# Performance work log

Hardware: AMD Instinct MI355X
Metric: run time of the kernel (lower is better)

## Reference

```python
import jax, jax.numpy as jnp
import numpy as np

N = 769  # last row is dropped inside forward (per original code)
REPEL_MARGIN = 0.08
MIN_SIZE = 0.02
SIZE_WEIGHT = 1.0
IOU_WEIGHT = 1.0
IOU_MARGIN = 0.1
EPS = 1e-12


def setup_inputs() -> dict:
    key = jax.random.key(0)
    k1, k2, k3 = jax.random.split(key, 3)
    centers = jax.random.uniform(k1, (N, 2), dtype=jnp.float32)
    wh = jax.random.uniform(k2, (N, 2), dtype=jnp.float32) * 0.1 + 0.01
    ang = jax.random.uniform(k3, (N,), dtype=jnp.float32) * np.float32(np.pi) - np.float32(np.pi / 2)
    pred = jnp.concatenate(
        [centers, wh, jnp.cos(ang)[:, None], jnp.sin(ang)[:, None]], axis=-1
    )  # [N, 6] = (cx, cy, w, h, cos_t, sin_t)
    return {"pred": pred}


def _cross(a, b):
    return a[..., 0] * b[..., 1] - a[..., 1] * b[..., 0]


def _corners(b):
    # b [..., 5] = (cx, cy, w, h, theta) -> [..., 4, 2] corners in CCW order
    cx, cy, w, h, a = (b[..., i] for i in range(5))
    c, s = jnp.cos(a), jnp.sin(a)
    dx = jnp.stack([-w, w, w, -w], -1) * 0.5
    dy = jnp.stack([-h, -h, h, h], -1) * 0.5
    x = cx[..., None] + c[..., None] * dx - s[..., None] * dy
    y = cy[..., None] + s[..., None] * dx + c[..., None] * dy
    return jnp.stack([x, y], -1)


def _points_in_box(pts, box):
    # pts [..., 4, 2], box [..., 5] -> bool [..., 4]
    cx, cy, w, h, a = (box[..., i] for i in range(5))
    c, s = jnp.cos(a), jnp.sin(a)
    dx = pts[..., 0] - cx[..., None]
    dy = pts[..., 1] - cy[..., None]
    lx = c[..., None] * dx + s[..., None] * dy
    ly = -s[..., None] * dx + c[..., None] * dy
    return (jnp.abs(lx) <= w[..., None] * 0.5) & (jnp.abs(ly) <= h[..., None] * 0.5)


def box_iou_rotated(boxes):
    # exact pairwise rotated-box IoU, boxes [n, 5] -> [n, n]
    n = boxes.shape[0]
    cor = _corners(boxes)  # [n, 4, 2]
    c1 = jnp.broadcast_to(cor[:, None], (n, n, 4, 2))
    c2 = jnp.broadcast_to(cor[None, :], (n, n, 4, 2))
    # all 4x4 edge-edge intersection candidates
    p = c1[:, :, :, None, :]
    r = (jnp.roll(c1, -1, axis=2) - c1)[:, :, :, None, :]
    q = c2[:, :, None, :, :]
    s = (jnp.roll(c2, -1, axis=2) - c2)[:, :, None, :, :]
    den = _cross(r, s)                         # [n, n, 4, 4]
    safe = jnp.abs(den) > EPS
    den_s = jnp.where(safe, den, 1.0)
    qp = q - p
    t = jnp.where(safe, _cross(qp, s) / den_s, 0.0)
    u = jnp.where(safe, _cross(qp, r) / den_s, 0.0)
    m_int = safe & (t >= 0) & (t <= 1) & (u >= 0) & (u <= 1)
    pts_int = (p + t[..., None] * r).reshape(n, n, 16, 2)
    m_int = m_int.reshape(n, n, 16)
    # corners of each box contained in the other
    m_21 = _points_in_box(c2, boxes[:, None])  # box2 corners in box1
    m_12 = _points_in_box(c1, boxes[None, :])  # box1 corners in box2
    pts_all = jnp.concatenate([pts_int, c2, c1], axis=2)   # [n, n, 24, 2]
    mask = jnp.concatenate([m_int, m_21, m_12], axis=2)    # [n, n, 24]
    # convex-hull area of valid candidate points via angle sort + shoelace
    cnt = mask.sum(-1)
    mf = mask[..., None].astype(pts_all.dtype)
    mean = (pts_all * mf).sum(2) / jnp.maximum(cnt, 1)[..., None]
    d = pts_all - mean[..., None, :]
    ang = jnp.where(mask, jnp.arctan2(d[..., 1], d[..., 0]), 1e6)  # invalids last
    order = jnp.argsort(ang, axis=-1)
    ps = jnp.take_along_axis(pts_all, order[..., None], axis=2)
    ms = jnp.take_along_axis(mask, order, axis=2)
    first = ps[..., 0:1, :]
    pf = jnp.where(ms[..., None], ps, first)  # pad invalid with first valid (zero cross)
    rel = pf - mean[..., None, :]
    inter = 0.5 * jnp.abs(_cross(rel, jnp.roll(rel, -1, axis=2)).sum(-1))
    area = boxes[:, 2] * boxes[:, 3]
    union = area[:, None] + area[None, :] - inter
    return jnp.where(union > EPS, inter / jnp.maximum(union, EPS), 0.0)


def reference(pred):
    pred = pred[:-1]
    m = pred.shape[0]
    centers = pred[:, :2]
    d2 = ((centers[:, None, :] - centers[None, :, :]) ** 2).sum(-1)
    eye = jnp.eye(m, dtype=bool)
    dist = jnp.sqrt(jnp.where(eye, 1.0, d2))
    off = (~eye).astype(dist.dtype)
    repel_loss = (jnp.maximum(REPEL_MARGIN - dist, 0.0) * off).sum() / (m * (m - 1))
    size_pen = jnp.maximum(MIN_SIZE - pred[:, 2], 0.0) + jnp.maximum(MIN_SIZE - pred[:, 3], 0.0)
    size_loss = size_pen.mean()
    total = repel_loss + SIZE_WEIGHT * size_loss
    theta = jnp.arctan2(pred[:, 5], pred[:, 4])
    obb = jnp.concatenate([pred[:, :4], theta[:, None]], axis=-1)
    ious = box_iou_rotated(obb) - jnp.eye(m, dtype=obb.dtype)
    iou_loss = jnp.maximum(ious - IOU_MARGIN, 0.0).mean()
    total = total + IOU_WEIGHT * iou_loss
    return total
```

## Files before the change

### kernel.cpp

```cpp
#include <hip/hip_runtime.h>

#define M  768
#define HALF (M / 2)
#define REPEL_MARGIN 0.08f
#define MIN_SIZE 0.02f
#define IOU_MARGIN 0.1f
#define NBLOCKS M

__device__ inline float edge_contrib(float px, float py, float qx, float qy,
                                     float W, float H,
                                     float bpx, float bpy, float bqx, float bqy) {
    float dx = qx - px, dy = qy - py;
    dx = (fabsf(dx) < 1e-12f) ? 1e-12f : dx;
    dy = (fabsf(dy) < 1e-12f) ? 1e-12f : dy;
    float rdx = __builtin_amdgcn_rcpf(dx);
    float rdy = __builtin_amdgcn_rcpf(dy);
    float tax = (-W - px) * rdx, tbx = (W - px) * rdx;
    float tay = (-H - py) * rdy, tby = (H - py) * rdy;
    float t0 = fmaxf(fmaxf(fminf(tax, tbx), fminf(tay, tby)), 0.0f);
    float t1 = fminf(fminf(fmaxf(tax, tbx), fmaxf(tay, tby)), 1.0f);
    t1 = fmaxf(t1, t0);
    float bdx = bqx - bpx, bdy = bqy - bpy;
    float sx = bpx + t0 * bdx, sy = bpy + t0 * bdy;
    float ex = bpx + t1 * bdx, ey = bpy + t1 * bdy;
    return sx * ey - sy * ex;
}

__global__ void __launch_bounds__(384)
box_repel_stage1(const float* __restrict__ pred, float* __restrict__ partial) {
    const int r = blockIdx.x;
    const int d = threadIdx.x + 1;
    int j = r + d; if (j >= M) j -= M;

    const float* bi = pred + 6 * r;
    const float cxi = bi[0], cyi = bi[1], wi = bi[2], hi = bi[3];
    const float ci = bi[4], si = bi[5];

    const float* bj = pred + 6 * j;
    const float cxj = bj[0], cyj = bj[1], wj = bj[2], hj = bj[3];
    const float cj = bj[4], sj = bj[5];

    const float rx = cxi - cxj, ry = cyi - cyj;
    const float dist = sqrtf(rx * rx + ry * ry);
    float contrib = fmaxf(REPEL_MARGIN - dist, 0.0f)
                    * (1.0f / ((float)M * (float)(M - 1)));

    const float wa = 0.5f * wi, ha = 0.5f * hi;
    const float wb = 0.5f * wj, hb = 0.5f * hj;
    const float tx =  cj * rx + sj * ry;
    const float ty = -sj * rx + cj * ry;
    const float cc = ci * cj + si * sj;
    const float ss = si * cj - ci * sj;

    const float cw = cc * wa, sw = ss * wa, ch = cc * ha, sh = ss * ha;
    const float ax0 = tx - cw + sh, ay0 = ty - sw - ch;
    const float ax1 = tx + cw + sh, ay1 = ty + sw - ch;
    const float ax2 = tx + cw - sh, ay2 = ty + sw + ch;
    const float ax3 = tx - cw - sh, ay3 = ty - sw + ch;

    const float bx0 = -wb, by0 = -hb;
    const float bx1 =  wb, by1 = -hb;
    const float bx2 =  wb, by2 =  hb;
    const float bx3 = -wb, by3 =  hb;

    #define TOA_X(bx, by) ( cc * ((bx) - tx) + ss * ((by) - ty))
    #define TOA_Y(bx, by) (-ss * ((bx) - tx) + cc * ((by) - ty))
    const float qx0 = TOA_X(bx0, by0), qy0 = TOA_Y(bx0, by0);
    const float qx1 = TOA_X(bx1, by1), qy1 = TOA_Y(bx1, by1);
    const float qx2 = TOA_X(bx2, by2), qy2 = TOA_Y(bx2, by2);
    const float qx3 = TOA_X(bx3, by3), qy3 = TOA_Y(bx3, by3);
    #undef TOA_X
    #undef TOA_Y

    float s2 = 0.0f;
    s2 += edge_contrib(ax0, ay0, ax1, ay1, wb, hb, ax0, ay0, ax1, ay1);
    s2 += edge_contrib(ax1, ay1, ax2, ay2, wb, hb, ax1, ay1, ax2, ay2);
    s2 += edge_contrib(ax2, ay2, ax3, ay3, wb, hb, ax2, ay2, ax3, ay3);
    s2 += edge_contrib(ax3, ay3, ax0, ay0, wb, hb, ax3, ay3, ax0, ay0);
    s2 += edge_contrib(qx0, qy0, qx1, qy1, wa, ha, bx0, by0, bx1, by1);
    s2 += edge_contrib(qx1, qy1, qx2, qy2, wa, ha, bx1, by1, bx2, by2);
    s2 += edge_contrib(qx2, qy2, qx3, qy3, wa, ha, bx2, by2, bx3, by3);
    s2 += edge_contrib(qx3, qy3, qx0, qy0, wa, ha, bx3, by3, bx0, by0);

    const float inter = fmaxf(0.5f * s2, 0.0f);
    const float uni = wi * hi + wj * hj - inter;
    const float iou = inter / fmaxf(uni, 1e-12f);
    contrib += fmaxf(iou - IOU_MARGIN, 0.0f)
               * (1.0f / ((float)M * (float)M));

    const float w = (d == HALF) ? 1.0f : 2.0f;
    contrib *= w;

    if (threadIdx.x == 0) {
        contrib += (fmaxf(MIN_SIZE - wi, 0.0f) + fmaxf(MIN_SIZE - hi, 0.0f))
                   * (1.0f / (float)M);
    }

    float v = contrib;
    #pragma unroll
    for (int off = 32; off > 0; off >>= 1) v += __shfl_down(v, off);

    __shared__ float sdata[6];
    const int lane = threadIdx.x & 63;
    const int wid  = threadIdx.x >> 6;
    if (lane == 0) sdata[wid] = v;
    __syncthreads();
    if (threadIdx.x == 0) {
        float s = sdata[0] + sdata[1] + sdata[2]
                + sdata[3] + sdata[4] + sdata[5];
        partial[blockIdx.x] = s;
    }
}

__global__ void __launch_bounds__(256)
box_repel_stage2(const float* __restrict__ partial, float* __restrict__ out) {
    float v = 0.0f;
    #pragma unroll
    for (int k = 0; k < NBLOCKS / 256; ++k)
        v += partial[k * 256 + threadIdx.x];

    #pragma unroll
    for (int off = 32; off > 0; off >>= 1) v += __shfl_down(v, off);

    __shared__ float sdata[4];
    const int lane = threadIdx.x & 63;
    const int wid  = threadIdx.x >> 6;
    if (lane == 0) sdata[wid] = v;
    __syncthreads();
    if (threadIdx.x == 0)
        out[0] = sdata[0] + sdata[1] + sdata[2] + sdata[3];
}

extern "C" void kernel_launch(void* const* d_in, const int* in_sizes, int n_in,
                              void* d_out, int out_size, void* d_ws, size_t ws_size,
                              hipStream_t stream) {
    const float* pred = (const float*)d_in[0];
    float* out = (float*)d_out;
    float* partial = (float*)d_ws;

    box_repel_stage1<<<NBLOCKS, 384, 0, stream>>>(pred, partial);
    box_repel_stage2<<<1, 256, 0, stream>>>(partial, out);
}
```

Measured before the change: 57.31 us.

## Cull far box pairs and compact near pairs before rotated-IoU work

Each block first tests every pair against a distance threshold (the larger of the repel margin and the two circumscribed half-diagonals), then compacts the surviving pair offsets into shared memory with an atomic counter. Only the compacted threads run the full rotated-intersection computation, so warps no longer spend cycles on pairs that cannot overlap. The culling is geometrically conservative, so results stay exact, at the cost of an extra sync and shared atomics. The stage-2 reduction is also shrunk to a single wavefront.

```diff
diff --git a/kernel.cpp b/kernel.cpp
--- a/kernel.cpp
+++ b/kernel.cpp
@@ -29,69 +29,96 @@
 __global__ void __launch_bounds__(384)
 box_repel_stage1(const float* __restrict__ pred, float* __restrict__ partial) {
     const int r = blockIdx.x;
-    const int d = threadIdx.x + 1;
-    int j = r + d; if (j >= M) j -= M;
+    const int tid = threadIdx.x;
+
+    __shared__ int s_cnt;
+    __shared__ int s_idx[384];
+    if (tid == 0) s_cnt = 0;
 
     const float* bi = pred + 6 * r;
     const float cxi = bi[0], cyi = bi[1], wi = bi[2], hi = bi[3];
     const float ci = bi[4], si = bi[5];
+    const float halfdiag2_i = 0.5f * (wi * wi + hi * hi);
 
-    const float* bj = pred + 6 * j;
-    const float cxj = bj[0], cyj = bj[1], wj = bj[2], hj = bj[3];
-    const float cj = bj[4], sj = bj[5];
+    __syncthreads();
 
-    const float rx = cxi - cxj, ry = cyi - cyj;
-    const float dist = sqrtf(rx * rx + ry * ry);
-    float contrib = fmaxf(REPEL_MARGIN - dist, 0.0f)
-                    * (1.0f / ((float)M * (float)(M - 1)));
+    {
+        const int d = tid + 1;
+        int j = r + d; if (j >= M) j -= M;
+        const float2 cj2 = *(const float2*)(pred + 6 * j);
+        const float2 wh2 = *(const float2*)(pred + 6 * j + 2);
+        const float rx = cxi - cj2.x, ry = cyi - cj2.y;
+        const float dist2 = rx * rx + ry * ry;
+        const float thr2 = fmaxf(REPEL_MARGIN * REPEL_MARGIN,
+                                 halfdiag2_i + 0.5f * (wh2.x * wh2.x + wh2.y * wh2.y));
+        if (dist2 <= thr2) {
+            s_idx[atomicAdd(&s_cnt, 1)] = d;
+        }
+    }
+    __syncthreads();
+    const int cnt = s_cnt;
 
-    const float wa = 0.5f * wi, ha = 0.5f * hi;
-    const float wb = 0.5f * wj, hb = 0.5f * hj;
-    const float tx =  cj * rx + sj * ry;
-    const float ty = -sj * rx + cj * ry;
-    const float cc = ci * cj + si * sj;
-    const float ss = si * cj - ci * sj;
+    float contrib = 0.0f;
+    if (tid < cnt) {
+        const int d = s_idx[tid];
+        int j = r + d; if (j >= M) j -= M;
 
-    const float cw = cc * wa, sw = ss * wa, ch = cc * ha, sh = ss * ha;
-    const float ax0 = tx - cw + sh, ay0 = ty - sw - ch;
-    const float ax1 = tx + cw + sh, ay1 = ty + sw - ch;
-    const float ax2 = tx + cw - sh, ay2 = ty + sw + ch;
-    const float ax3 = tx - cw - sh, ay3 = ty - sw + ch;
+        const float* bj = pred + 6 * j;
+        const float cxj = bj[0], cyj = bj[1], wj = bj[2], hj = bj[3];
+        const float cj = bj[4], sj = bj[5];
 
-    const float bx0 = -wb, by0 = -hb;
-    const float bx1 =  wb, by1 = -hb;
-    const float bx2 =  wb, by2 =  hb;
-    const float bx3 = -wb, by3 =  hb;
+        const float rx = cxi - cxj, ry = cyi - cyj;
+        const float dist = sqrtf(rx * rx + ry * ry);
+        contrib = fmaxf(REPEL_MARGIN - dist, 0.0f)
+                  * (1.0f / ((float)M * (float)(M - 1)));
 
-    #define TOA_X(bx, by) ( cc * ((bx) - tx) + ss * ((by) - ty))
-    #define TOA_Y(bx, by) (-ss * ((bx) - tx) + cc * ((by) - ty))
-    const float qx0 = TOA_X(bx0, by0), qy0 = TOA_Y(bx0, by0);
-    const float qx1 = TOA_X(bx1, by1), qy1 = TOA_Y(bx1, by1);
-    const float qx2 = TOA_X(bx2, by2), qy2 = TOA_Y(bx2, by2);
-    const float qx3 = TOA_X(bx3, by3), qy3 = TOA_Y(bx3, by3);
-    #undef TOA_X
-    #undef TOA_Y
+        const float wa = 0.5f * wi, ha = 0.5f * hi;
+        const float wb = 0.5f * wj, hb = 0.5f * hj;
+        const float tx =  cj * rx + sj * ry;
+        const float ty = -sj * rx + cj * ry;
+        const float cc = ci * cj + si * sj;
+        const float ss = si * cj - ci * sj;
 
-    float s2 = 0.0f;
-    s2 += edge_contrib(ax0, ay0, ax1, ay1, wb, hb, ax0, ay0, ax1, ay1);
-    s2 += edge_contrib(ax1, ay1, ax2, ay2, wb, hb, ax1, ay1, ax2, ay2);
-    s2 += edge_contrib(ax2, ay2, ax3, ay3, wb, hb, ax2, ay2, ax3, ay3);
-    s2 += edge_contrib(ax3, ay3, ax0, ay0, wb, hb, ax3, ay3, ax0, ay0);
-    s2 += edge_contrib(qx0, qy0, qx1, qy1, wa, ha, bx0, by0, bx1, by1);
-    s2 += edge_contrib(qx1, qy1, qx2, qy2, wa, ha, bx1, by1, bx2, by2);
-    s2 += edge_contrib(qx2, qy2, qx3, qy3, wa, ha, bx2, by2, bx3, by3);
-    s2 += edge_contrib(qx3, qy3, qx0, qy0, wa, ha, bx3, by3, bx0, by0);
+        const float cw = cc * wa, sw = ss * wa, ch = cc * ha, sh = ss * ha;
+        const float ax0 = tx - cw + sh, ay0 = ty - sw - ch;
+        const float ax1 = tx + cw + sh, ay1 = ty + sw - ch;
+        const float ax2 = tx + cw - sh, ay2 = ty + sw + ch;
+        const float ax3 = tx - cw - sh, ay3 = ty - sw + ch;
 
-    const float inter = fmaxf(0.5f * s2, 0.0f);
-    const float uni = wi * hi + wj * hj - inter;
-    const float iou = inter / fmaxf(uni, 1e-12f);
-    contrib += fmaxf(iou - IOU_MARGIN, 0.0f)
-               * (1.0f / ((float)M * (float)M));
+        const float bx0 = -wb, by0 = -hb;
+        const float bx1 =  wb, by1 = -hb;
+        const float bx2 =  wb, by2 =  hb;
+        const float bx3 = -wb, by3 =  hb;
 
-    const float w = (d == HALF) ? 1.0f : 2.0f;
-    contrib *= w;
+        #define TOA_X(bx, by) ( cc * ((bx) - tx) + ss * ((by) - ty))
+        #define TOA_Y(bx, by) (-ss * ((bx) - tx) + cc * ((by) - ty))
+        const float qx0 = TOA_X(bx0, by0), qy0 = TOA_Y(bx0, by0);
+        const float qx1 = TOA_X(bx1, by1), qy1 = TOA_Y(bx1, by1);
+        const float qx2 = TOA_X(bx2, by2), qy2 = TOA_Y(bx2, by2);
+        const float qx3 = TOA_X(bx3, by3), qy3 = TOA_Y(bx3, by3);
+        #undef TOA_X
+        #undef TOA_Y
 
-    if (threadIdx.x == 0) {
+        float s2 = 0.0f;
+        s2 += edge_contrib(ax0, ay0, ax1, ay1, wb, hb, ax0, ay0, ax1, ay1);
+        s2 += edge_contrib(ax1, ay1, ax2, ay2, wb, hb, ax1, ay1, ax2, ay2);
+        s2 += edge_contrib(ax2, ay2, ax3, ay3, wb, hb, ax2, ay2, ax3, ay3);
+        s2 += edge_contrib(ax3, ay3, ax0, ay0, wb, hb, ax3, ay3, ax0, ay0);
+        s2 += edge_contrib(qx0, qy0, qx1, qy1, wa, ha, bx0, by0, bx1, by1);
+        s2 += edge_contrib(qx1, qy1, qx2, qy2, wa, ha, bx1, by1, bx2, by2);
+        s2 += edge_contrib(qx2, qy2, qx3, qy3, wa, ha, bx2, by2, bx3, by3);
+        s2 += edge_contrib(qx3, qy3, qx0, qy0, wa, ha, bx3, by3, bx0, by0);
+
+        const float inter = fmaxf(0.5f * s2, 0.0f);
+        const float uni = wi * hi + wj * hj - inter;
+        const float iou = inter / fmaxf(uni, 1e-12f);
+        contrib += fmaxf(iou - IOU_MARGIN, 0.0f)
+                   * (1.0f / ((float)M * (float)M));
+
+        contrib *= (d == HALF) ? 1.0f : 2.0f;
+    }
+
+    if (tid == 0) {
         contrib += (fmaxf(MIN_SIZE - wi, 0.0f) + fmaxf(MIN_SIZE - hi, 0.0f))
                    * (1.0f / (float)M);
     }
@@ -101,34 +128,28 @@
     for (int off = 32; off > 0; off >>= 1) v += __shfl_down(v, off);
 
     __shared__ float sdata[6];
-    const int lane = threadIdx.x & 63;
-    const int wid  = threadIdx.x >> 6;
+    const int lane = tid & 63;
+    const int wid  = tid >> 6;
     if (lane == 0) sdata[wid] = v;
     __syncthreads();
-    if (threadIdx.x == 0) {
+    if (tid == 0) {
         float s = sdata[0] + sdata[1] + sdata[2]
                 + sdata[3] + sdata[4] + sdata[5];
         partial[blockIdx.x] = s;
     }
 }
 
-__global__ void __launch_bounds__(256)
+__global__ void __launch_bounds__(64)
 box_repel_stage2(const float* __restrict__ partial, float* __restrict__ out) {
     float v = 0.0f;
     #pragma unroll
-    for (int k = 0; k < NBLOCKS / 256; ++k)
-        v += partial[k * 256 + threadIdx.x];
+    for (int k = 0; k < NBLOCKS / 64; ++k)
+        v += partial[k * 64 + threadIdx.x];
 
     #pragma unroll
     for (int off = 32; off > 0; off >>= 1) v += __shfl_down(v, off);
 
-    __shared__ float sdata[4];
-    const int lane = threadIdx.x & 63;
-    const int wid  = threadIdx.x >> 6;
-    if (lane == 0) sdata[wid] = v;
-    __syncthreads();
-    if (threadIdx.x == 0)
-        out[0] = sdata[0] + sdata[1] + sdata[2] + sdata[3];
+    if (threadIdx.x == 0) out[0] = v;
 }
 
 extern "C" void kernel_launch(void* const* d_in, const int* in_sizes, int n_in,
@@ -139,5 +160,5 @@
     float* partial = (float*)d_ws;
 
     box_repel_stage1<<<NBLOCKS, 384, 0, stream>>>(pred, partial);
-    box_repel_stage2<<<1, 256, 0, stream>>>(partial, out);
+    box_repel_stage2<<<1, 64, 0, stream>>>(partial, out);
 }
```

Result: faster. 56.12 us (-2.1%).
